# Kernel tuning notes

Measured on AMD Instinct MI355X. Metric: run time of the kernel, lower is better.

Reference implementation:

```python
import jax, jax.numpy as jnp
import numpy as np

ENC_HID = 512
DEC_HID = 512


def setup_inputs() -> dict:
    key = jax.random.key(0)
    k1, k2, k3, k4, k5 = jax.random.split(key, 5)
    hidden = jax.random.normal(k1, (64, DEC_HID), dtype=jnp.float32)
    encoder_outputs = jax.random.normal(k2, (1024, 64, 2 * ENC_HID), dtype=jnp.float32)
    in_dim = 2 * ENC_HID + DEC_HID
    # Linear params (stored as [in, out] for x @ W + b)
    scale = 1.0 / np.sqrt(in_dim)
    W = jax.random.uniform(k3, (in_dim, DEC_HID), dtype=jnp.float32, minval=-scale, maxval=scale)
    b = jax.random.uniform(k4, (DEC_HID,), dtype=jnp.float32, minval=-scale, maxval=scale)
    v = jax.random.uniform(k5, (DEC_HID,), dtype=jnp.float32)  # torch.rand in [0,1)
    return {"hidden": hidden, "encoder_outputs": encoder_outputs, "W": W, "b": b, "v": v}


def reference(hidden, encoder_outputs, W, b, v):
    # hidden: [B, Dd]; encoder_outputs: [S, B, 2*De]
    src_len = encoder_outputs.shape[0]
    enc = jnp.transpose(encoder_outputs, (1, 0, 2))            # [B, S, 2*De]
    hid = jnp.broadcast_to(hidden[:, None, :], (hidden.shape[0], src_len, hidden.shape[1]))  # [B, S, Dd]
    concat = jnp.concatenate([hid, enc], axis=2)               # [B, S, Dd+2*De]
    energy = jnp.tanh(concat @ W + b)                          # [B, S, Dd]
    scores = jnp.einsum("bsd,d->bs", energy, v)                # [B, S]
    return jax.nn.softmax(scores, axis=1)
```

## Files before the change

kernel.cpp:

```cpp
#include <hip/hip_runtime.h>
#include <stdint.h>


typedef float  floatx4 __attribute__((ext_vector_type(4)));
typedef __bf16 bf16x8  __attribute__((ext_vector_type(8)));
typedef short  short8  __attribute__((ext_vector_type(8)));

union bfu  { bf16x8 v; short8 s; };

#define LOG2E_X2 2.8853900817779268f

#define BAR()                                              \
  do {                                                     \
    asm volatile("s_waitcnt lgkmcnt(0)" ::: "memory");     \
    __builtin_amdgcn_sched_barrier(0);                     \
    __builtin_amdgcn_s_barrier();                          \
    __builtin_amdgcn_sched_barrier(0);                     \
  } while (0)

#define SB() __builtin_amdgcn_sched_barrier(0)

__global__ void wt_convert(const float* __restrict__ W, __bf16* __restrict__ Bp) {
  __shared__ float tile[64][65];
  const int kt = blockIdx.x >> 3;
  const int nt = blockIdx.x & 7;
  const int c  = threadIdx.x & 63;
  const int r4 = threadIdx.x >> 6;
  #pragma unroll 4
  for (int i = 0; i < 16; i++) {
    int r = i * 4 + r4;
    tile[r][c] = W[(long)(512 + kt * 64 + r) * 512 + nt * 64 + c];
  }
  __syncthreads();
  const int n_loc = threadIdx.x & 63;
  const int kc4   = threadIdx.x >> 6;
  const int n_g   = nt * 64 + n_loc;
  const int wc    = n_g >> 7;
  const int ct    = (n_g >> 4) & 7;
  const int t     = n_g & 15;
  #pragma unroll
  for (int i = 0; i < 2; i++) {
    int chunk = i * 4 + kc4;
    int k_g   = kt * 64 + chunk * 8;
    int T     = k_g >> 5;
    int q     = (k_g >> 3) & 3;
    union bfu u;
    #pragma unroll
    for (int j = 0; j < 8; j++) u.v[j] = (__bf16)tile[chunk * 8 + j][n_loc];
    long cidx = ((long)(T * 4 + wc) * 8 + ct) * 64 + q * 16 + t;
    *(bf16x8*)(Bp + cidx * 8) = u.v;
  }
}

__global__ void hproj_kernel(const float* __restrict__ hidden,
                             const float* __restrict__ W,
                             const float* __restrict__ bias,
                             float* __restrict__ hproj) {
  const int tid = threadIdx.x;
  const int b_  = blockIdx.x >> 2;
  const int kc  = blockIdx.x & 3;
  __shared__ float hid[128];
  if (tid < 128) hid[tid] = hidden[b_ * 512 + kc * 128 + tid];
  __syncthreads();
  float acc = (kc == 0) ? bias[tid] : 0.f;
  const float* Wp = W + (long)(kc * 128) * 512 + tid;
  #pragma unroll 8
  for (int k = 0; k < 128; k++) acc = fmaf(hid[k], Wp[(long)k * 512], acc);
  atomicAdd(&hproj[b_ * 512 + tid], acc);
}

__global__ __launch_bounds__(512, 2) void gemm_score(
    const float* __restrict__ enc,
    const __bf16* __restrict__ Bp,
    const float* __restrict__ hproj,
    const float* __restrict__ v,
    float* __restrict__ scores)
{
  __shared__ __bf16 ldsA[2][4096];
  __shared__ float bscore[128];

  const int tid  = threadIdx.x;
  const int lane = tid & 63;
  const int wv   = tid >> 6;
  const int wc   = wv & 3;
  const int wr   = wv >> 2;
  const int q    = lane >> 4;
  const int t    = lane & 15;
  const long m0  = (long)blockIdx.x * 128;

  const int sm = tid >> 2;
  const int sf = tid & 3;
  const float* ap = enc + (m0 + sm) * 1024 + sf * 8;
  __bf16* aw0 = &ldsA[0][sf * 1024 + ((sm * 8) ^ (sf * 16))];
  __bf16* aw1 = &ldsA[1][sf * 1024 + ((sm * 8) ^ (sf * 16))];

  const __bf16* ar0 = &ldsA[0][q * 1024 + wr * 512 + ((t * 8) ^ (q * 16))];
  const __bf16* ar1 = &ldsA[1][q * 1024 + wr * 512 + ((t * 8) ^ (q * 16))];

  const __bf16* bpb = Bp + (long)wc * 4096 + (long)lane * 8;

  if (tid < 128) bscore[tid] = 0.f;

  floatx4 acc[4][8];
  #pragma unroll
  for (int i = 0; i < 4; i++)
    #pragma unroll
    for (int j = 0; j < 8; j++)
      acc[i][j] = (floatx4){0.f, 0.f, 0.f, 0.f};

  floatx4 ra[3][2];
  short8  bfr[2][8];

  auto issueA = [&](int T, int s) {
    const float* p = ap + T * 32;
    ra[s][0] = *(const floatx4*)(p);
    ra[s][1] = *(const floatx4*)(p + 4);
  };
  auto writeA = [&](int s, __bf16* dst) {
    union bfu u;
    #pragma unroll
    for (int j = 0; j < 4; j++) {
      u.v[j]     = (__bf16)ra[s][0][j];
      u.v[4 + j] = (__bf16)ra[s][1][j];
    }
    *(bf16x8*)dst = u.v;
  };
  auto loadB = [&](int T, int s) {
    #pragma unroll
    for (int ct = 0; ct < 8; ct++) {
      union bfu u;
      u.v = *(const bf16x8*)(bpb + (long)T * 16384 + ct * 512);
      bfr[s][ct] = u.s;
    }
  };
  auto compute = [&](const __bf16* base, int bs) {
    #pragma unroll
    for (int rt = 0; rt < 4; rt++) {
      union bfu u;
      u.v = *(const bf16x8*)(base + rt * 128);
      #pragma unroll
      for (int ct = 0; ct < 8; ct++)
        acc[rt][ct] = __builtin_amdgcn_mfma_f32_16x16x32_bf16(
            u.s, bfr[bs][ct], acc[rt][ct], 0, 0, 0);
    }
  };

  issueA(0, 0); issueA(1, 1); issueA(2, 2);
  loadB(0, 0);  loadB(1, 1);
  writeA(0, aw0);
  BAR();

#define PHASE(T)                                           \
  {                                                        \
    compute(((T) & 1) ? ar1 : ar0, (T) & 1);               \
    SB();                                                  \
    if ((T) < 31) writeA(((T) + 1) % 3, ((T) & 1) ? aw0 : aw1); \
    if ((T) < 30) loadB((T) + 2, (T) & 1);                 \
    SB();                                                  \
    if ((T) < 29) issueA((T) + 3, (T) % 3);                \
    BAR();                                                 \
  }

  PHASE(0)  PHASE(1)  PHASE(2)  PHASE(3)
  PHASE(4)  PHASE(5)  PHASE(6)  PHASE(7)
  PHASE(8)  PHASE(9)  PHASE(10) PHASE(11)
  PHASE(12) PHASE(13) PHASE(14) PHASE(15)
  PHASE(16) PHASE(17) PHASE(18) PHASE(19)
  PHASE(20) PHASE(21) PHASE(22) PHASE(23)
  PHASE(24) PHASE(25) PHASE(26) PHASE(27)
  PHASE(28) PHASE(29) PHASE(30) PHASE(31)
#undef PHASE

  float vv[8];
  #pragma unroll
  for (int ct = 0; ct < 8; ct++) vv[ct] = v[wc * 128 + ct * 16 + t];

  #pragma unroll
  for (int rt = 0; rt < 4; rt++) {
    #pragma unroll
    for (int r = 0; r < 4; r++) {
      int row = wr * 64 + rt * 16 + q * 4 + r;
      const float* hrow = hproj + (row & 63) * 512 + wc * 128 + t;
      float s = 0.f;
      #pragma unroll
      for (int ct = 0; ct < 8; ct++) {
        float e  = acc[rt][ct][r] + hrow[ct * 16];
        float ex = __builtin_amdgcn_exp2f(e * LOG2E_X2);
        float th = 1.f - 2.f * __builtin_amdgcn_rcpf(ex + 1.f);
        s = fmaf(vv[ct], th, s);
      }
      s += __shfl_xor(s, 1);
      s += __shfl_xor(s, 2);
      s += __shfl_xor(s, 4);
      s += __shfl_xor(s, 8);
      if (t == 0) atomicAdd(&bscore[row], s);
    }
  }
  __syncthreads();
  if (tid < 128)
    scores[(long)(tid & 63) * 1024 + blockIdx.x * 2 + (tid >> 6)] = bscore[tid];
}

__global__ void softmax_kernel(const float* __restrict__ scores,
                               float* __restrict__ out) {
  const int b_   = blockIdx.x;
  const int tid  = threadIdx.x;
  const int lane = tid & 63;
  const int wv   = tid >> 6;
  __shared__ float redmax[4], redsum[4];

  float x[4];
  #pragma unroll
  for (int i = 0; i < 4; i++) x[i] = scores[b_ * 1024 + i * 256 + tid];
  float mx = fmaxf(fmaxf(x[0], x[1]), fmaxf(x[2], x[3]));
  #pragma unroll
  for (int off = 1; off < 64; off <<= 1) mx = fmaxf(mx, __shfl_xor(mx, off));
  if (lane == 0) redmax[wv] = mx;
  __syncthreads();
  mx = fmaxf(fmaxf(redmax[0], redmax[1]), fmaxf(redmax[2], redmax[3]));

  float e[4], s = 0.f;
  #pragma unroll
  for (int i = 0; i < 4; i++) { e[i] = __expf(x[i] - mx); s += e[i]; }
  #pragma unroll
  for (int off = 1; off < 64; off <<= 1) s += __shfl_xor(s, off);
  if (lane == 0) redsum[wv] = s;
  __syncthreads();
  s = redsum[0] + redsum[1] + redsum[2] + redsum[3];
  float inv = 1.f / s;
  #pragma unroll
  for (int i = 0; i < 4; i++) out[b_ * 1024 + i * 256 + tid] = e[i] * inv;
}

extern "C" void kernel_launch(void* const* d_in, const int* in_sizes, int n_in,
                              void* d_out, int out_size, void* d_ws, size_t ws_size,
                              hipStream_t stream) {
  (void)in_sizes; (void)n_in; (void)out_size; (void)ws_size;
  const float* hidden = (const float*)d_in[0];
  const float* enc    = (const float*)d_in[1];
  const float* W      = (const float*)d_in[2];
  const float* bias   = (const float*)d_in[3];
  const float* v      = (const float*)d_in[4];
  float* out = (float*)d_out;

  char* ws = (char*)d_ws;
  __bf16* Bp    = (__bf16*)ws;
  float*  hproj = (float*)(ws + (1 << 20));
  float*  scores= (float*)(ws + (1 << 20) + (128 << 10));

  hipMemsetAsync(hproj, 0, 64 * 512 * sizeof(float), stream);
  wt_convert<<<128, 256, 0, stream>>>(W, Bp);
  hproj_kernel<<<256, 512, 0, stream>>>(hidden, W, bias, hproj);
  gemm_score<<<512, 512, 0, stream>>>(enc, Bp, hproj, v, scores);
  softmax_kernel<<<64, 256, 0, stream>>>(scores, out);
}
```

Measured before the change: 430.2 us.

## Pre-pack encoder outputs to bf16 MFMA layout in separate kernel, drop LDS staging

Adds a kernel that converts the fp32 encoder outputs into a bf16 buffer already arranged in the MFMA fragment order. The GEMM then loads A fragments straight from global memory into registers, with no LDS staging and no barriers. The block shrinks to 4 waves covering 64 rows, and twice as many blocks are launched. The aim is to remove LDS traffic and barrier stalls from the main loop, at the price of an extra full pass that writes and re-reads a 64MB bf16 copy of the input.

```diff
diff --git a/kernel.cpp b/kernel.cpp
--- a/kernel.cpp
+++ b/kernel.cpp
@@ -3,21 +3,13 @@
 
 
 typedef float  floatx4 __attribute__((ext_vector_type(4)));
+typedef __bf16 bf16x4  __attribute__((ext_vector_type(4)));
 typedef __bf16 bf16x8  __attribute__((ext_vector_type(8)));
 typedef short  short8  __attribute__((ext_vector_type(8)));
 
-union bfu  { bf16x8 v; short8 s; };
+union bfu { bf16x8 v; short8 s; };
 
 #define LOG2E_X2 2.8853900817779268f
-
-#define BAR()                                              \
-  do {                                                     \
-    asm volatile("s_waitcnt lgkmcnt(0)" ::: "memory");     \
-    __builtin_amdgcn_sched_barrier(0);                     \
-    __builtin_amdgcn_s_barrier();                          \
-    __builtin_amdgcn_sched_barrier(0);                     \
-  } while (0)
-
 #define SB() __builtin_amdgcn_sched_barrier(0)
 
 __global__ void wt_convert(const float* __restrict__ W, __bf16* __restrict__ Bp) {
@@ -69,37 +61,58 @@
   atomicAdd(&hproj[b_ * 512 + tid], acc);
 }
 
-__global__ __launch_bounds__(512, 2) void gemm_score(
-    const float* __restrict__ enc,
+__global__ void aconv_kernel(const float* __restrict__ enc,
+                             __bf16* __restrict__ Apack) {
+  __shared__ __bf16 lds16[16][1026];
+  const int R  = blockIdx.x;
+  const int u  = threadIdx.x;
+  const int rl = u >> 4;
+  const int cb = u & 15;
+  const int l  = u & 63;
+  const int w4 = u >> 6;
+  const int q  = l >> 4, t = l & 15;
+  for (int s3 = 0; s3 < 4; s3++) {
+    const float* src = enc + ((long)(R * 64 + s3 * 16 + rl)) * 1024 + cb * 4;
+    #pragma unroll
+    for (int i = 0; i < 16; i++) {
+      floatx4 v4 = *(const floatx4*)(src + i * 64);
+      bf16x4 b4;
+      b4[0] = (__bf16)v4[0]; b4[1] = (__bf16)v4[1];
+      b4[2] = (__bf16)v4[2]; b4[3] = (__bf16)v4[3];
+      *(bf16x4*)(&lds16[rl][cb * 4 + i * 64]) = b4;
+    }
+    __syncthreads();
+    #pragma unroll
+    for (int i = 0; i < 8; i++) {
+      int T = i * 4 + w4;
+      bf16x8 val = *(const bf16x8*)(&lds16[t][T * 32 + q * 8]);
+      *(bf16x8*)(Apack + (((long)(R * 32 + T) * 4 + s3) * 64 + l) * 8) = val;
+    }
+    __syncthreads();
+  }
+}
+
+__global__ __launch_bounds__(256, 2) void gemm_score(
+    const __bf16* __restrict__ Apack,
     const __bf16* __restrict__ Bp,
     const float* __restrict__ hproj,
     const float* __restrict__ v,
     float* __restrict__ scores)
 {
-  __shared__ __bf16 ldsA[2][4096];
-  __shared__ float bscore[128];
+  __shared__ float bscore[64];
 
   const int tid  = threadIdx.x;
   const int lane = tid & 63;
-  const int wv   = tid >> 6;
-  const int wc   = wv & 3;
-  const int wr   = wv >> 2;
+  const int wc   = tid >> 6;
   const int q    = lane >> 4;
   const int t    = lane & 15;
-  const long m0  = (long)blockIdx.x * 128;
-
-  const int sm = tid >> 2;
-  const int sf = tid & 3;
-  const float* ap = enc + (m0 + sm) * 1024 + sf * 8;
-  __bf16* aw0 = &ldsA[0][sf * 1024 + ((sm * 8) ^ (sf * 16))];
-  __bf16* aw1 = &ldsA[1][sf * 1024 + ((sm * 8) ^ (sf * 16))];
-
-  const __bf16* ar0 = &ldsA[0][q * 1024 + wr * 512 + ((t * 8) ^ (q * 16))];
-  const __bf16* ar1 = &ldsA[1][q * 1024 + wr * 512 + ((t * 8) ^ (q * 16))];
-
-  const __bf16* bpb = Bp + (long)wc * 4096 + (long)lane * 8;
-
-  if (tid < 128) bscore[tid] = 0.f;
+
+  if (tid < 64) bscore[tid] = 0.f;
+  __syncthreads();
+
+  const __bf16* apb = Apack + ((long)blockIdx.x * 128 + lane) * 8 * 16;
+  const __bf16* apbase = Apack + (long)blockIdx.x * 32 * 4 * 512 + (long)lane * 8;
+  const __bf16* bpbase = Bp + (long)wc * 4096 + (long)lane * 8;
 
   floatx4 acc[4][8];
   #pragma unroll
@@ -108,57 +121,42 @@
     for (int j = 0; j < 8; j++)
       acc[i][j] = (floatx4){0.f, 0.f, 0.f, 0.f};
 
-  floatx4 ra[3][2];
-  short8  bfr[2][8];
-
-  auto issueA = [&](int T, int s) {
-    const float* p = ap + T * 32;
-    ra[s][0] = *(const floatx4*)(p);
-    ra[s][1] = *(const floatx4*)(p + 4);
-  };
-  auto writeA = [&](int s, __bf16* dst) {
-    union bfu u;
-    #pragma unroll
-    for (int j = 0; j < 4; j++) {
-      u.v[j]     = (__bf16)ra[s][0][j];
-      u.v[4 + j] = (__bf16)ra[s][1][j];
-    }
-    *(bf16x8*)dst = u.v;
-  };
-  auto loadB = [&](int T, int s) {
+  short8 afr[2][4];
+  short8 bfr[2][8];
+
+  auto issueP = [&](int T, int s) {
+    #pragma unroll
+    for (int rt = 0; rt < 4; rt++) {
+      union bfu u;
+      u.v = *(const bf16x8*)(apbase + ((long)T * 4 + rt) * 512);
+      afr[s][rt] = u.s;
+    }
     #pragma unroll
     for (int ct = 0; ct < 8; ct++) {
       union bfu u;
-      u.v = *(const bf16x8*)(bpb + (long)T * 16384 + ct * 512);
+      u.v = *(const bf16x8*)(bpbase + (long)T * 16384 + ct * 512);
       bfr[s][ct] = u.s;
     }
   };
-  auto compute = [&](const __bf16* base, int bs) {
-    #pragma unroll
-    for (int rt = 0; rt < 4; rt++) {
-      union bfu u;
-      u.v = *(const bf16x8*)(base + rt * 128);
+  auto computeP = [&](int s) {
+    #pragma unroll
+    for (int rt = 0; rt < 4; rt++)
       #pragma unroll
       for (int ct = 0; ct < 8; ct++)
         acc[rt][ct] = __builtin_amdgcn_mfma_f32_16x16x32_bf16(
-            u.s, bfr[bs][ct], acc[rt][ct], 0, 0, 0);
-    }
+            afr[s][rt], bfr[s][ct], acc[rt][ct], 0, 0, 0);
   };
 
-  issueA(0, 0); issueA(1, 1); issueA(2, 2);
-  loadB(0, 0);  loadB(1, 1);
-  writeA(0, aw0);
-  BAR();
+  (void)apb;
+  issueP(0, 0);
+  issueP(1, 1);
 
 #define PHASE(T)                                           \
   {                                                        \
-    compute(((T) & 1) ? ar1 : ar0, (T) & 1);               \
+    computeP((T) & 1);                                     \
     SB();                                                  \
-    if ((T) < 31) writeA(((T) + 1) % 3, ((T) & 1) ? aw0 : aw1); \
-    if ((T) < 30) loadB((T) + 2, (T) & 1);                 \
+    if ((T) < 30) issueP((T) + 2, (T) & 1);                \
     SB();                                                  \
-    if ((T) < 29) issueA((T) + 3, (T) % 3);                \
-    BAR();                                                 \
   }
 
   PHASE(0)  PHASE(1)  PHASE(2)  PHASE(3)
@@ -179,8 +177,8 @@
   for (int rt = 0; rt < 4; rt++) {
     #pragma unroll
     for (int r = 0; r < 4; r++) {
-      int row = wr * 64 + rt * 16 + q * 4 + r;
-      const float* hrow = hproj + (row & 63) * 512 + wc * 128 + t;
+      int row = rt * 16 + q * 4 + r;
+      const float* hrow = hproj + row * 512 + wc * 128 + t;
       float s = 0.f;
       #pragma unroll
       for (int ct = 0; ct < 8; ct++) {
@@ -197,8 +195,7 @@
     }
   }
   __syncthreads();
-  if (tid < 128)
-    scores[(long)(tid & 63) * 1024 + blockIdx.x * 2 + (tid >> 6)] = bscore[tid];
+  if (tid < 64) scores[(long)tid * 1024 + blockIdx.x] = bscore[tid];
 }
 
 __global__ void softmax_kernel(const float* __restrict__ scores,
@@ -247,10 +244,12 @@
   __bf16* Bp    = (__bf16*)ws;
   float*  hproj = (float*)(ws + (1 << 20));
   float*  scores= (float*)(ws + (1 << 20) + (128 << 10));
+  __bf16* Apack = (__bf16*)(ws + (2 << 20));
 
   hipMemsetAsync(hproj, 0, 64 * 512 * sizeof(float), stream);
   wt_convert<<<128, 256, 0, stream>>>(W, Bp);
   hproj_kernel<<<256, 512, 0, stream>>>(hidden, W, bias, hproj);
-  gemm_score<<<512, 512, 0, stream>>>(enc, Bp, hproj, v, scores);
+  aconv_kernel<<<1024, 256, 0, stream>>>(enc, Apack);
+  gemm_score<<<1024, 256, 0, stream>>>(Apack, Bp, hproj, v, scores);
   softmax_kernel<<<64, 256, 0, stream>>>(scores, out);
 }
```

Measured after the change: 485.7 us. 12.9% more time.

## Stage fp32 encoder tiles via async global-to-LDS loads with deep ring buffer

Applied to the files above, without the earlier changes.

The GEMM kernel now copies fp32 encoder rows straight into LDS with global_load_lds into an 8-deep ring buffer (7 stages in flight), using an XOR swizzle. The bf16 conversion moves to the LDS read side. Blocks shrink to 64 rows and 4 waves (1024 blocks of 256 threads), each wave covering 128 output columns. The aim is to remove the register round trip and the per-phase LDS writes and to keep more memory requests in flight. In exchange, LDS use per block doubles because it holds fp32 (64 KB), fewer waves share each B fragment load, and the vmcnt accounting has to stay exactly right.

```diff
diff --git a/kernel.cpp b/kernel.cpp
--- a/kernel.cpp
+++ b/kernel.cpp
@@ -6,19 +6,24 @@
 typedef __bf16 bf16x8  __attribute__((ext_vector_type(8)));
 typedef short  short8  __attribute__((ext_vector_type(8)));
 
-union bfu  { bf16x8 v; short8 s; };
+union bfu { bf16x8 v; short8 s; };
 
 #define LOG2E_X2 2.8853900817779268f
+#define SB() __builtin_amdgcn_sched_barrier(0)
 
 #define BAR()                                              \
   do {                                                     \
     asm volatile("s_waitcnt lgkmcnt(0)" ::: "memory");     \
-    __builtin_amdgcn_sched_barrier(0);                     \
+    SB();                                                  \
     __builtin_amdgcn_s_barrier();                          \
-    __builtin_amdgcn_sched_barrier(0);                     \
+    SB();                                                  \
   } while (0)
 
-#define SB() __builtin_amdgcn_sched_barrier(0)
+__device__ __forceinline__ void async_ld16(const void* g, void* l) {
+  __builtin_amdgcn_global_load_lds(
+      (const __attribute__((address_space(1))) void*)g,
+      (__attribute__((address_space(3))) void*)l, 16, 0, 0);
+}
 
 __global__ void wt_convert(const float* __restrict__ W, __bf16* __restrict__ Bp) {
   __shared__ float tile[64][65];
@@ -69,37 +74,33 @@
   atomicAdd(&hproj[b_ * 512 + tid], acc);
 }
 
-__global__ __launch_bounds__(512, 2) void gemm_score(
+__global__ __launch_bounds__(256) void gemm_score(
     const float* __restrict__ enc,
     const __bf16* __restrict__ Bp,
     const float* __restrict__ hproj,
     const float* __restrict__ v,
     float* __restrict__ scores)
 {
-  __shared__ __bf16 ldsA[2][4096];
-  __shared__ float bscore[128];
+  __shared__ float ldsA[8][2048];
+  __shared__ float bscore[64];
 
   const int tid  = threadIdx.x;
   const int lane = tid & 63;
-  const int wv   = tid >> 6;
-  const int wc   = wv & 3;
-  const int wr   = wv >> 2;
+  const int wc   = tid >> 6;
   const int q    = lane >> 4;
   const int t    = lane & 15;
-  const long m0  = (long)blockIdx.x * 128;
-
-  const int sm = tid >> 2;
-  const int sf = tid & 3;
-  const float* ap = enc + (m0 + sm) * 1024 + sf * 8;
-  __bf16* aw0 = &ldsA[0][sf * 1024 + ((sm * 8) ^ (sf * 16))];
-  __bf16* aw1 = &ldsA[1][sf * 1024 + ((sm * 8) ^ (sf * 16))];
-
-  const __bf16* ar0 = &ldsA[0][q * 1024 + wr * 512 + ((t * 8) ^ (q * 16))];
-  const __bf16* ar1 = &ldsA[1][q * 1024 + wr * 512 + ((t * 8) ^ (q * 16))];
+  const long m0  = (long)blockIdx.x * 64;
+
+  const int r0 = tid >> 3, s0 = tid & 7;
+  const int r1 = r0 + 32;
+  const float* src0 = enc + (m0 + r0) * 1024 + ((s0 ^ (r0 & 7)) << 2);
+  const float* src1 = enc + (m0 + r1) * 1024 + ((s0 ^ (r1 & 7)) << 2);
+  const int d0 = tid * 4;
+  const int d1 = 1024 + tid * 4;
 
   const __bf16* bpb = Bp + (long)wc * 4096 + (long)lane * 8;
 
-  if (tid < 128) bscore[tid] = 0.f;
+  if (tid < 64) bscore[tid] = 0.f;
 
   floatx4 acc[4][8];
   #pragma unroll
@@ -108,22 +109,12 @@
     for (int j = 0; j < 8; j++)
       acc[i][j] = (floatx4){0.f, 0.f, 0.f, 0.f};
 
-  floatx4 ra[3][2];
-  short8  bfr[2][8];
-
-  auto issueA = [&](int T, int s) {
-    const float* p = ap + T * 32;
-    ra[s][0] = *(const floatx4*)(p);
-    ra[s][1] = *(const floatx4*)(p + 4);
-  };
-  auto writeA = [&](int s, __bf16* dst) {
-    union bfu u;
-    #pragma unroll
-    for (int j = 0; j < 4; j++) {
-      u.v[j]     = (__bf16)ra[s][0][j];
-      u.v[4 + j] = (__bf16)ra[s][1][j];
-    }
-    *(bf16x8*)dst = u.v;
+  short8 bfr[2][8];
+
+  auto stage = [&](int T) {
+    float* db = &ldsA[T & 7][0];
+    async_ld16(src0 + T * 32, db + d0);
+    async_ld16(src1 + T * 32, db + d1);
   };
   auto loadB = [&](int T, int s) {
     #pragma unroll
@@ -133,11 +124,19 @@
       bfr[s][ct] = u.s;
     }
   };
-  auto compute = [&](const __bf16* base, int bs) {
+  auto compute = [&](int T, int bs) {
+    const float* bb = &ldsA[T & 7][0];
     #pragma unroll
     for (int rt = 0; rt < 4; rt++) {
+      const int r = rt * 16 + t;
+      floatx4 f0 = *(const floatx4*)(bb + r * 32 + (((2 * q)     ^ (t & 7)) << 2));
+      floatx4 f1 = *(const floatx4*)(bb + r * 32 + (((2 * q + 1) ^ (t & 7)) << 2));
       union bfu u;
-      u.v = *(const bf16x8*)(base + rt * 128);
+      #pragma unroll
+      for (int j = 0; j < 4; j++) {
+        u.v[j]     = (__bf16)f0[j];
+        u.v[4 + j] = (__bf16)f1[j];
+      }
       #pragma unroll
       for (int ct = 0; ct < 8; ct++)
         acc[rt][ct] = __builtin_amdgcn_mfma_f32_16x16x32_bf16(
@@ -145,20 +144,19 @@
     }
   };
 
-  issueA(0, 0); issueA(1, 1); issueA(2, 2);
-  loadB(0, 0);  loadB(1, 1);
-  writeA(0, aw0);
-  BAR();
+  stage(0); stage(1); stage(2); stage(3); stage(4); stage(5); stage(6);
+  loadB(0, 0); loadB(1, 1);
+  asm volatile("s_waitcnt vmcnt(16)" ::: "memory");
+  SB();
+  __builtin_amdgcn_s_barrier();
+  SB();
 
 #define PHASE(T)                                           \
   {                                                        \
-    compute(((T) & 1) ? ar1 : ar0, (T) & 1);               \
-    SB();                                                  \
-    if ((T) < 31) writeA(((T) + 1) % 3, ((T) & 1) ? aw0 : aw1); \
+    if ((T) > 0) BAR();                                    \
+    if ((T) < 25) stage((T) + 7);                          \
+    compute((T), (T) & 1);                                 \
     if ((T) < 30) loadB((T) + 2, (T) & 1);                 \
-    SB();                                                  \
-    if ((T) < 29) issueA((T) + 3, (T) % 3);                \
-    BAR();                                                 \
   }
 
   PHASE(0)  PHASE(1)  PHASE(2)  PHASE(3)
@@ -179,8 +177,8 @@
   for (int rt = 0; rt < 4; rt++) {
     #pragma unroll
     for (int r = 0; r < 4; r++) {
-      int row = wr * 64 + rt * 16 + q * 4 + r;
-      const float* hrow = hproj + (row & 63) * 512 + wc * 128 + t;
+      int row = rt * 16 + q * 4 + r;
+      const float* hrow = hproj + row * 512 + wc * 128 + t;
       float s = 0.f;
       #pragma unroll
       for (int ct = 0; ct < 8; ct++) {
@@ -197,8 +195,7 @@
     }
   }
   __syncthreads();
-  if (tid < 128)
-    scores[(long)(tid & 63) * 1024 + blockIdx.x * 2 + (tid >> 6)] = bscore[tid];
+  if (tid < 64) scores[(long)tid * 1024 + blockIdx.x] = bscore[tid];
 }
 
 __global__ void softmax_kernel(const float* __restrict__ scores,
@@ -251,6 +248,6 @@
   hipMemsetAsync(hproj, 0, 64 * 512 * sizeof(float), stream);
   wt_convert<<<128, 256, 0, stream>>>(W, Bp);
   hproj_kernel<<<256, 512, 0, stream>>>(hidden, W, bias, hproj);
-  gemm_score<<<512, 512, 0, stream>>>(enc, Bp, hproj, v, scores);
+  gemm_score<<<1024, 256, 0, stream>>>(enc, Bp, hproj, v, scores);
   softmax_kernel<<<64, 256, 0, stream>>>(scores, out);
 }
```

Result: slower. 470.9 us (+9.5%).

## Shrink GEMM tile to 32 rows with 4 waves and 2048 blocks

Applied to the files above, without the earlier changes.

Reduces the gemm_score block tile from 128 rows and 8 waves to 32 rows and 4 waves, launching 2048 blocks instead of 512. B fragments are now single-buffered. The aim is more parallelism and occupancy across the CUs and less register pressure. The cost is that every 32-row block reloads the full B weight matrix, which raises L2 traffic per unit of work and cuts B reuse.

```diff
diff --git a/kernel.cpp b/kernel.cpp
--- a/kernel.cpp
+++ b/kernel.cpp
@@ -3,10 +3,12 @@
 
 
 typedef float  floatx4 __attribute__((ext_vector_type(4)));
+typedef __bf16 bf16x4  __attribute__((ext_vector_type(4)));
 typedef __bf16 bf16x8  __attribute__((ext_vector_type(8)));
 typedef short  short8  __attribute__((ext_vector_type(8)));
 
 union bfu  { bf16x8 v; short8 s; };
+union bfu4 { bf16x4 v; uint2 u; };
 
 #define LOG2E_X2 2.8853900817779268f
 
@@ -69,93 +71,88 @@
   atomicAdd(&hproj[b_ * 512 + tid], acc);
 }
 
-__global__ __launch_bounds__(512, 2) void gemm_score(
+__global__ __launch_bounds__(256) void gemm_score(
     const float* __restrict__ enc,
     const __bf16* __restrict__ Bp,
     const float* __restrict__ hproj,
     const float* __restrict__ v,
     float* __restrict__ scores)
 {
-  __shared__ __bf16 ldsA[2][4096];
-  __shared__ float bscore[128];
+  __shared__ __bf16 ldsA[2][1024];
+  __shared__ float bscore[32];
 
   const int tid  = threadIdx.x;
   const int lane = tid & 63;
-  const int wv   = tid >> 6;
-  const int wc   = wv & 3;
-  const int wr   = wv >> 2;
+  const int wc   = tid >> 6;
   const int q    = lane >> 4;
   const int t    = lane & 15;
-  const long m0  = (long)blockIdx.x * 128;
-
-  const int sm = tid >> 2;
-  const int sf = tid & 3;
-  const float* ap = enc + (m0 + sm) * 1024 + sf * 8;
-  __bf16* aw0 = &ldsA[0][sf * 1024 + ((sm * 8) ^ (sf * 16))];
-  __bf16* aw1 = &ldsA[1][sf * 1024 + ((sm * 8) ^ (sf * 16))];
-
-  const __bf16* ar0 = &ldsA[0][q * 1024 + wr * 512 + ((t * 8) ^ (q * 16))];
-  const __bf16* ar1 = &ldsA[1][q * 1024 + wr * 512 + ((t * 8) ^ (q * 16))];
+  const long m0  = (long)blockIdx.x * 32;
+
+  const int m  = tid >> 3;
+  const int kq = tid & 7;
+  const int c_ = kq >> 1;
+  const int jh = (kq & 1) * 4;
+  const float* ap = enc + (m0 + m) * 1024 + kq * 4;
+  __bf16* aw0 = &ldsA[0][c_ * 256 + ((m * 8) ^ (c_ * 16)) + jh];
+  __bf16* aw1 = &ldsA[1][c_ * 256 + ((m * 8) ^ (c_ * 16)) + jh];
+
+  const __bf16* ar0 = &ldsA[0][q * 256 + ((t * 8) ^ (q * 16))];
+  const __bf16* ar1 = &ldsA[1][q * 256 + ((t * 8) ^ (q * 16))];
 
   const __bf16* bpb = Bp + (long)wc * 4096 + (long)lane * 8;
 
-  if (tid < 128) bscore[tid] = 0.f;
-
-  floatx4 acc[4][8];
-  #pragma unroll
-  for (int i = 0; i < 4; i++)
+  if (tid < 32) bscore[tid] = 0.f;
+
+  floatx4 acc[2][8];
+  #pragma unroll
+  for (int i = 0; i < 2; i++)
     #pragma unroll
     for (int j = 0; j < 8; j++)
       acc[i][j] = (floatx4){0.f, 0.f, 0.f, 0.f};
 
-  floatx4 ra[3][2];
-  short8  bfr[2][8];
+  floatx4 ra[3];
+  short8  bfr[8];
 
   auto issueA = [&](int T, int s) {
-    const float* p = ap + T * 32;
-    ra[s][0] = *(const floatx4*)(p);
-    ra[s][1] = *(const floatx4*)(p + 4);
+    ra[s] = *(const floatx4*)(ap + T * 32);
   };
   auto writeA = [&](int s, __bf16* dst) {
-    union bfu u;
-    #pragma unroll
-    for (int j = 0; j < 4; j++) {
-      u.v[j]     = (__bf16)ra[s][0][j];
-      u.v[4 + j] = (__bf16)ra[s][1][j];
-    }
-    *(bf16x8*)dst = u.v;
-  };
-  auto loadB = [&](int T, int s) {
+    union bfu4 u;
+    #pragma unroll
+    for (int j = 0; j < 4; j++) u.v[j] = (__bf16)ra[s][j];
+    *(bf16x4*)dst = u.v;
+  };
+  auto loadB = [&](int T) {
     #pragma unroll
     for (int ct = 0; ct < 8; ct++) {
       union bfu u;
       u.v = *(const bf16x8*)(bpb + (long)T * 16384 + ct * 512);
-      bfr[s][ct] = u.s;
+      bfr[ct] = u.s;
     }
   };
-  auto compute = [&](const __bf16* base, int bs) {
-    #pragma unroll
-    for (int rt = 0; rt < 4; rt++) {
+  auto compute = [&](const __bf16* base) {
+    #pragma unroll
+    for (int rt = 0; rt < 2; rt++) {
       union bfu u;
       u.v = *(const bf16x8*)(base + rt * 128);
       #pragma unroll
       for (int ct = 0; ct < 8; ct++)
         acc[rt][ct] = __builtin_amdgcn_mfma_f32_16x16x32_bf16(
-            u.s, bfr[bs][ct], acc[rt][ct], 0, 0, 0);
+            u.s, bfr[ct], acc[rt][ct], 0, 0, 0);
     }
   };
 
   issueA(0, 0); issueA(1, 1); issueA(2, 2);
-  loadB(0, 0);  loadB(1, 1);
+  loadB(0);
   writeA(0, aw0);
   BAR();
 
 #define PHASE(T)                                           \
   {                                                        \
-    compute(((T) & 1) ? ar1 : ar0, (T) & 1);               \
+    compute(((T) & 1) ? ar1 : ar0);                        \
     SB();                                                  \
     if ((T) < 31) writeA(((T) + 1) % 3, ((T) & 1) ? aw0 : aw1); \
-    if ((T) < 30) loadB((T) + 2, (T) & 1);                 \
+    if ((T) < 31) loadB((T) + 1);                          \
     SB();                                                  \
     if ((T) < 29) issueA((T) + 3, (T) % 3);                \
     BAR();                                                 \
@@ -175,12 +172,13 @@
   #pragma unroll
   for (int ct = 0; ct < 8; ct++) vv[ct] = v[wc * 128 + ct * 16 + t];
 
-  #pragma unroll
-  for (int rt = 0; rt < 4; rt++) {
+  const int bbase = (blockIdx.x & 1) * 32;
+  #pragma unroll
+  for (int rt = 0; rt < 2; rt++) {
     #pragma unroll
     for (int r = 0; r < 4; r++) {
-      int row = wr * 64 + rt * 16 + q * 4 + r;
-      const float* hrow = hproj + (row & 63) * 512 + wc * 128 + t;
+      int row = rt * 16 + q * 4 + r;
+      const float* hrow = hproj + (bbase + row) * 512 + wc * 128 + t;
       float s = 0.f;
       #pragma unroll
       for (int ct = 0; ct < 8; ct++) {
@@ -197,8 +195,8 @@
     }
   }
   __syncthreads();
-  if (tid < 128)
-    scores[(long)(tid & 63) * 1024 + blockIdx.x * 2 + (tid >> 6)] = bscore[tid];
+  if (tid < 32)
+    scores[(long)(bbase + tid) * 1024 + (blockIdx.x >> 1)] = bscore[tid];
 }
 
 __global__ void softmax_kernel(const float* __restrict__ scores,
@@ -251,6 +249,6 @@
   hipMemsetAsync(hproj, 0, 64 * 512 * sizeof(float), stream);
   wt_convert<<<128, 256, 0, stream>>>(W, Bp);
   hproj_kernel<<<256, 512, 0, stream>>>(hidden, W, bias, hproj);
-  gemm_score<<<512, 512, 0, stream>>>(enc, Bp, hproj, v, scores);
+  gemm_score<<<2048, 256, 0, stream>>>(enc, Bp, hproj, v, scores);
   softmax_kernel<<<64, 256, 0, stream>>>(scores, out);
 }
```

After: 468.9 us. 1.09x slower.
